# Kernel tuning notes

Hardware: AMD Instinct MI355X
Metric: run time of the kernel (lower is better)

Reference implementation:

```python
import jax, jax.numpy as jnp
import numpy as np

B, C, H, W = 4, 256, 64, 64
RED = 8
DQK = C // RED  # 32


def setup_inputs() -> dict:
    key = jax.random.key(0)
    ks = jax.random.split(key, 8)
    x = jax.random.normal(ks[0], (B, C, H, W), dtype=jnp.float32)
    # 1x1 conv weights == per-pixel linear maps: [out_ch, in_ch] + bias [out_ch]
    q_w = jax.random.normal(ks[1], (DQK, C), dtype=jnp.float32) * (1.0 / np.sqrt(C))
    q_b = jax.random.normal(ks[2], (DQK,), dtype=jnp.float32) * 0.01
    k_w = jax.random.normal(ks[3], (DQK, C), dtype=jnp.float32) * (1.0 / np.sqrt(C))
    k_b = jax.random.normal(ks[4], (DQK,), dtype=jnp.float32) * 0.01
    v_w = jax.random.normal(ks[5], (C, C), dtype=jnp.float32) * (1.0 / np.sqrt(C))
    v_b = jax.random.normal(ks[6], (C,), dtype=jnp.float32) * 0.01
    # gamma is init'd to 0 in torch; use a nonzero value so the attention path matters
    gamma = jax.random.normal(ks[7], (1,), dtype=jnp.float32) * 0.1
    return {"x": x, "q_w": q_w, "q_b": q_b, "k_w": k_w, "k_b": k_b,
            "v_w": v_w, "v_b": v_b, "gamma": gamma}


def reference(x, q_w, q_b, k_w, k_b, v_w, v_b, gamma):
    b, c, h, w = x.shape
    xf = x.reshape(b, c, h * w)  # [B, C, N]
    # 1x1 convs as channel matmuls
    q = jnp.einsum('dc,bcn->bdn', q_w, xf) + q_b[None, :, None]  # [B, DQK, N]
    k = jnp.einsum('dc,bcn->bdn', k_w, xf) + k_b[None, :, None]  # [B, DQK, N]
    v = jnp.einsum('oc,bcn->bon', v_w, xf) + v_b[None, :, None]  # [B, C, N]
    # attn[b, n, m] = softmax_m( q[:,n] . k[:,m] )  -- NO 1/sqrt(d) scale (faithful)
    scores = jnp.einsum('bdn,bdm->bnm', q, k)  # [B, N, N]
    attn = jax.nn.softmax(scores, axis=-1)
    # out = v @ attn^T : out[b, c, n] = sum_m v[b, c, m] * attn[b, n, m]
    out = jnp.einsum('bcm,bnm->bcn', v, attn).reshape(b, c, h, w)
    return gamma[0] * out + x
```

## Files before the change

kernel.cpp:

```cpp
#include <hip/hip_runtime.h>

#define NN 4096
#define CC 256
#define DQ 32

typedef __attribute__((ext_vector_type(8))) short short8;
typedef __attribute__((ext_vector_type(4))) float f32x4;

__device__ __forceinline__ unsigned short f32_to_bf16(float f) {
  unsigned int u = __float_as_uint(f);
  u += 0x7fffu + ((u >> 16) & 1u);
  return (unsigned short)(u >> 16);
}

__device__ __forceinline__ float bf16_to_f32(unsigned short u) {
  return __uint_as_float(((unsigned int)u) << 16);
}

__device__ __forceinline__ float exp2_hw(float f) {
  return __builtin_amdgcn_exp2f(f);
}

__device__ __forceinline__ unsigned cvt_pk_bf16(float lo, float hi) {
  unsigned r;
  asm("v_cvt_pk_bf16_f32 %0, %1, %2" : "=v"(r) : "v"(lo), "v"(hi));
  return r;
}

__device__ __forceinline__ void gld16(const void* g, void* l) {
  __builtin_amdgcn_global_load_lds(
      (__attribute__((address_space(1))) void*)(g),
      (__attribute__((address_space(3))) void*)(l), 16, 0, 0);
}

__global__ __launch_bounds__(256) void wconv_kernel(
    const float* qw, const float* kw, const float* vw,
    const float* qb, const float* kb, const float* vb,
    unsigned short* Wcat, float* bcat) {
  int id = blockIdx.x * 256 + threadIdx.x;
  if (id < 320 * 256) {
    int row = id >> 8;
    float v;
    if (row < 32) v = qw[id];
    else if (row < 64) v = kw[id - 32 * 256];
    else v = vw[id - 64 * 256];
    Wcat[id] = f32_to_bf16(v);
  }
  if (id < 320) {
    float v;
    if (id < 32) v = qb[id];
    else if (id < 64) v = kb[id - 32];
    else v = vb[id - 64];
    bcat[id] = v;
  }
}

__global__ __launch_bounds__(256, 2) void proj_kernel(
    const float* x, const unsigned short* Wcat, const float* bcat,
    unsigned short* Qt, unsigned short* Kt, unsigned short* V) {
  int bid = blockIdx.x;
  int b = bid >> 7, nb = bid & 127;
  int tid = threadIdx.x, lane = tid & 63, w = tid >> 6;
  int l15 = lane & 15, h = lane >> 4;

  __shared__ unsigned short xT[32][272];
  __shared__ unsigned short vbuf[CC][32];
  {
    const float* xb = x + (size_t)b * CC * NN + nb * 32;
    int c0 = tid >> 3, n4 = (tid & 7) * 4;
#pragma unroll
    for (int i = 0; i < 8; i++) {
      int c = c0 + i * 32;
      f32x4 v = *(const f32x4*)(xb + (size_t)c * NN + n4);
#pragma unroll
      for (int j = 0; j < 4; j++) xT[n4 + j][c] = f32_to_bf16(v[j]);
    }
  }
  __syncthreads();

  short8 af0[8], af1[8];
#pragma unroll
  for (int ks = 0; ks < 8; ks++) {
    af0[ks] = *(const short8*)(&xT[l15][ks * 32 + h * 8]);
    af1[ks] = *(const short8*)(&xT[16 + l15][ks * 32 + h * 8]);
  }

  f32x4 acc0[5], acc1[5];
#pragma unroll
  for (int t = 0; t < 5; t++)
#pragma unroll
    for (int r = 0; r < 4; r++) { acc0[t][r] = 0.f; acc1[t][r] = 0.f; }

#pragma unroll
  for (int ks = 0; ks < 8; ks++) {
#pragma unroll
    for (int d = 0; d < 5; d++) {
      int dt = w * 5 + d;
      short8 bfr = *(const short8*)(Wcat + (size_t)(dt * 16 + l15) * CC + ks * 32 + h * 8);
      acc0[d] = __builtin_amdgcn_mfma_f32_16x16x32_bf16(af0[ks], bfr, acc0[d], 0, 0, 0);
      acc1[d] = __builtin_amdgcn_mfma_f32_16x16x32_bf16(af1[ks], bfr, acc1[d], 0, 0, 0);
    }
  }

  unsigned short* Qtb = Qt + (size_t)b * NN * DQ;
  unsigned short* Ktb = Kt + (size_t)b * NN * DQ;
#pragma unroll
  for (int d = 0; d < 5; d++) {
    int dt = w * 5 + d;
    float bias = bcat[dt * 16 + l15];
    if (dt < 4) {
      float scale = dt < 2 ? 1.44269504f : 1.0f;
      unsigned short* dst = dt < 2 ? Qtb : Ktb;
      int dd = (dt & 1) * 16 + l15;
#pragma unroll
      for (int r = 0; r < 4; r++) {
        int nA = nb * 32 + h * 4 + r;
        dst[(size_t)nA * DQ + dd] = f32_to_bf16((acc0[d][r] + bias) * scale);
        dst[(size_t)(nA + 16) * DQ + dd] = f32_to_bf16((acc1[d][r] + bias) * scale);
      }
    } else {
      int c = (dt - 4) * 16 + l15;
#pragma unroll
      for (int r = 0; r < 4; r++) {
        vbuf[c][h * 4 + r] = f32_to_bf16(acc0[d][r] + bias);
        vbuf[c][16 + h * 4 + r] = f32_to_bf16(acc1[d][r] + bias);
      }
    }
  }
  __syncthreads();
  unsigned short* Vb = V + (size_t)b * CC * NN + nb * 32;
  int c = tid;
#pragma unroll
  for (int k = 0; k < 4; k++)
    *(f32x4*)(Vb + (size_t)c * NN + k * 8) = *(const f32x4*)(&vbuf[c][k * 8]);
}

__global__ __launch_bounds__(1024, 4) void attn_kernel(
    const unsigned short* Qt, const unsigned short* Kt, const unsigned short* V,
    unsigned short* Apart, float* rspart) {
  int bid = blockIdx.x;
  int b  = (bid & 7) >> 1;
  int mh = bid & 1;
  int nb = bid >> 3;
  int tid = threadIdx.x, lane = tid & 63, w = tid >> 6;
  int grp = w >> 3, wq = w & 7, wc = w & 3, ntb = (w >> 2) & 1;
  int l15 = lane & 15, h = lane >> 4;
  int n0 = nb * 128 + wq * 16;
  int m0base = mh * 2048;

  const unsigned short* Qtb = Qt + (size_t)b * NN * DQ;
  const unsigned short* Ktb = Kt + (size_t)b * NN * DQ;
  const unsigned short* Vb  = V  + (size_t)b * CC * NN;

  __shared__ __align__(16) char ldsb[139264];

  short8 qf = *(const short8*)(Qtb + (size_t)(n0 + l15) * DQ + h * 8);

  f32x4 acc[16];
#pragma unroll
  for (int t = 0; t < 16; t++)
#pragma unroll
    for (int r = 0; r < 4; r++) acc[t][r] = 0.f;
  float rs = 0.f;

  f32x4 zero4;
#pragma unroll
  for (int r = 0; r < 4; r++) zero4[r] = 0.f;

  auto stage_to = [&](char* dst, int T) {
    int m0 = m0base + T * 64;
#pragma unroll
    for (int it = 0; it < 2; it++) {
      int idx = it * 1024 + tid;
      int c = idx >> 3, sub = idx & 7;
      int moff = (sub ^ (c & 7)) * 8;
      gld16(Vb + (size_t)c * NN + m0 + moff, dst + idx * 16);
    }
  };

  short8 kA[2];
  auto kload = [&](int T) {
    int m0 = m0base + T * 64 + grp * 32;
#pragma unroll
    for (int s = 0; s < 2; s++)
      kA[s] = *(const short8*)(Ktb + (size_t)(m0 + s * 16 + l15) * DQ + h * 8);
  };

  auto pvstep = [&](const char* vb2, const char* prd) {
    const char* pb = prd + (grp * 8 + ntb * 4) * 1280 + l15 * 80 + h * 16;
    short8 pf0 = *(const short8*)(pb + 0 * 1280);
    short8 pf1 = *(const short8*)(pb + 1 * 1280);
    short8 pf2 = *(const short8*)(pb + 2 * 1280);
    short8 pf3 = *(const short8*)(pb + 3 * 1280);
#pragma unroll
    for (int ct = 0; ct < 4; ct++) {
      int c = wc * 64 + ct * 16 + l15;
      int sub = (grp * 4 + h) ^ (c & 7);
      short8 vf = *(const short8*)(vb2 + c * 128 + sub * 16);
      acc[ct * 4 + 0] = __builtin_amdgcn_mfma_f32_16x16x32_bf16(vf, pf0, acc[ct * 4 + 0], 0, 0, 0);
      acc[ct * 4 + 1] = __builtin_amdgcn_mfma_f32_16x16x32_bf16(vf, pf1, acc[ct * 4 + 1], 0, 0, 0);
      acc[ct * 4 + 2] = __builtin_amdgcn_mfma_f32_16x16x32_bf16(vf, pf2, acc[ct * 4 + 2], 0, 0, 0);
      acc[ct * 4 + 3] = __builtin_amdgcn_mfma_f32_16x16x32_bf16(vf, pf3, acc[ct * 4 + 3], 0, 0, 0);
    }
  };

  char* vpv  = ldsb + 2 * 32768;
  char* vrdy = ldsb + 0 * 32768;
  char* vstg = ldsb + 1 * 32768;
  char* pbw  = ldsb + 98304;
  char* pbr  = ldsb + 98304 + 20480;

  stage_to(vrdy, 0);
  kload(0);

  for (int T = 0; T < 32; T++) {
    if (T + 1 < 32) stage_to(vstg, T + 1);
    f32x4 st0 = __builtin_amdgcn_mfma_f32_16x16x32_bf16(kA[0], qf, zero4, 0, 0, 0);
    f32x4 st1 = __builtin_amdgcn_mfma_f32_16x16x32_bf16(kA[1], qf, zero4, 0, 0, 0);
    if (T + 1 < 32) kload(T + 1);
    if (T > 0) pvstep(vpv, pbr);
    float e0 = exp2_hw(st0[0]), e1 = exp2_hw(st0[1]);
    float e2 = exp2_hw(st0[2]), e3 = exp2_hw(st0[3]);
    float f0 = exp2_hw(st1[0]), f1 = exp2_hw(st1[1]);
    float f2 = exp2_hw(st1[2]), f3 = exp2_hw(st1[3]);
    rs += ((e0 + e1) + (e2 + e3)) + ((f0 + f1) + (f2 + f3));
    int2 q0, q1;
    q0.x = (int)cvt_pk_bf16(e0, e1); q0.y = (int)cvt_pk_bf16(e2, e3);
    q1.x = (int)cvt_pk_bf16(f0, f1); q1.y = (int)cvt_pk_bf16(f2, f3);
    {
      char* pw = pbw + w * 1280 + l15 * 80 + h * 8;
      *(int2*)(pw + 0)  = q0;
      *(int2*)(pw + 32) = q1;
    }
    asm volatile("s_waitcnt lgkmcnt(0)" ::: "memory");
    __builtin_amdgcn_s_barrier();
    asm volatile("" ::: "memory");
    char* t0 = vpv; vpv = vrdy; vrdy = vstg; vstg = t0;
    char* t1 = pbw; pbw = pbr; pbr = t1;
  }
  pvstep(vpv, pbr);

  rs += __shfl_xor(rs, 16);
  rs += __shfl_xor(rs, 32);
  if (h == 0)
    rspart[(size_t)(b * 4 + mh * 2 + grp) * NN + nb * 128 + wq * 16 + l15] = rs;

  __syncthreads();
  char* pregion = ldsb + 98304;
#pragma unroll
  for (int r = 0; r < 4; r++) {
    if (grp == 1) {
#pragma unroll
      for (int i = 0; i < 4; i++)
        *(f32x4*)(pregion + (w - 8) * 4096 + i * 1024 + lane * 16) = acc[r * 4 + i];
    }
    __syncthreads();
    if (grp == 0) {
#pragma unroll
      for (int i = 0; i < 4; i++) {
        f32x4 p = *(const f32x4*)(pregion + w * 4096 + i * 1024 + lane * 16);
#pragma unroll
        for (int q = 0; q < 4; q++) acc[r * 4 + i][q] += p[q];
      }
    }
    __syncthreads();
  }

  unsigned short* ldsus = (unsigned short*)ldsb;
  if (grp == 0) {
#pragma unroll
    for (int ct = 0; ct < 4; ct++)
#pragma unroll
      for (int i = 0; i < 4; i++)
#pragma unroll
        for (int r = 0; r < 4; r++) {
          int c = wc * 64 + ct * 16 + h * 4 + r;
          int n = (ntb * 4 + i) * 16 + l15;
          ldsus[c * 128 + n] = f32_to_bf16(acc[ct * 4 + i][r]);
        }
  }
  __syncthreads();
  {
    unsigned short* Adst = Apart + (size_t)(b * 2 + mh) * CC * NN + nb * 128;
    int c = tid >> 2, seg = tid & 3;
    const f32x4* src = (const f32x4*)(ldsb + c * 256 + seg * 64);
#pragma unroll
    for (int k = 0; k < 4; k++)
      *(f32x4*)(Adst + (size_t)c * NN + seg * 32 + k * 8) = src[k];
  }
}

__global__ __launch_bounds__(256) void fuse_kernel(
    const unsigned short* Apart, const float* rspart, const float* x,
    const float* gamma, float* out) {
  int bid = blockIdx.x;
  int b = bid >> 9, c = (bid >> 1) & 255, half = bid & 1;
  int n0 = half * 2048 + threadIdx.x * 8;

  short8 a0 = *(const short8*)(Apart + ((size_t)(b * 2 + 0) * CC + c) * NN + n0);
  short8 a1 = *(const short8*)(Apart + ((size_t)(b * 2 + 1) * CC + c) * NN + n0);

  const float* rp = rspart + (size_t)b * 4 * NN + n0;
  f32x4 rlo, rhi;
#pragma unroll
  for (int q = 0; q < 4; q++) { rlo[q] = 0.f; rhi[q] = 0.f; }
#pragma unroll
  for (int p = 0; p < 4; p++) {
    f32x4 ra = *(const f32x4*)(rp + (size_t)p * NN);
    f32x4 rb = *(const f32x4*)(rp + (size_t)p * NN + 4);
#pragma unroll
    for (int q = 0; q < 4; q++) { rlo[q] += ra[q]; rhi[q] += rb[q]; }
  }

  const float* xp = x + ((size_t)b * CC + c) * NN + n0;
  f32x4 x0 = *(const f32x4*)(xp), x1 = *(const f32x4*)(xp + 4);
  float g = gamma[0];

  f32x4 o0, o1;
#pragma unroll
  for (int q = 0; q < 4; q++) {
    float a = bf16_to_f32((unsigned short)a0[q]) + bf16_to_f32((unsigned short)a1[q]);
    o0[q] = g * a / rlo[q] + x0[q];
    float a2 = bf16_to_f32((unsigned short)a0[q + 4]) + bf16_to_f32((unsigned short)a1[q + 4]);
    o1[q] = g * a2 / rhi[q] + x1[q];
  }
  float* op = out + ((size_t)b * CC + c) * NN + n0;
  *(f32x4*)op = o0;
  *(f32x4*)(op + 4) = o1;
}

extern "C" void kernel_launch(void* const* d_in, const int* in_sizes, int n_in,
                              void* d_out, int out_size, void* d_ws, size_t ws_size,
                              hipStream_t stream) {
  (void)in_sizes; (void)n_in; (void)out_size; (void)ws_size;
  const float* x  = (const float*)d_in[0];
  const float* qw = (const float*)d_in[1];
  const float* qb = (const float*)d_in[2];
  const float* kw = (const float*)d_in[3];
  const float* kb = (const float*)d_in[4];
  const float* vw = (const float*)d_in[5];
  const float* vb = (const float*)d_in[6];
  const float* gamma = (const float*)d_in[7];
  float* out = (float*)d_out;

  char* ws = (char*)d_ws;
  unsigned short* Wcat  = (unsigned short*)(ws);
  float*          bcat  = (float*)(ws + 163840);
  unsigned short* Qt    = (unsigned short*)(ws + 165120);
  unsigned short* Kt    = (unsigned short*)(ws + 1213696);
  unsigned short* V     = (unsigned short*)(ws + 2262272);
  unsigned short* Apart = (unsigned short*)(ws + 10650880);
  float*          rsprt = (float*)(ws + 27428096);

  hipLaunchKernelGGL(wconv_kernel, dim3(320), dim3(256), 0, stream,
                     qw, kw, vw, qb, kb, vb, Wcat, bcat);
  hipLaunchKernelGGL(proj_kernel, dim3(512), dim3(256), 0, stream,
                     x, Wcat, bcat, Qt, Kt, V);
  hipLaunchKernelGGL(attn_kernel, dim3(256), dim3(1024), 0, stream,
                     Qt, Kt, V, Apart, rsprt);
  hipLaunchKernelGGL(fuse_kernel, dim3(2048), dim3(256), 0, stream,
                     Apart, rsprt, x, gamma, out);
}
```

Baseline: 96.48 us.

## Stage K tiles through LDS with async triple-buffering and swizzle P buffer

K fragments, previously read from global memory straight into registers each iteration, are now loaded asynchronously into a triple-buffered LDS ring two tiles ahead and then read from LDS. The P buffer drops its 80-byte padded rows for 64-byte rows with an XOR swizzle, and the PV step moves after the P write, with explicit vmcnt waits. The intent is to hide global K latency and avoid LDS bank conflicts at a smaller footprint. In exchange it uses more LDS and adds LDS reads plus precise wait-count bookkeeping.

```diff
diff --git a/kernel.cpp b/kernel.cpp
--- a/kernel.cpp
+++ b/kernel.cpp
@@ -152,7 +152,7 @@
   const unsigned short* Ktb = Kt + (size_t)b * NN * DQ;
   const unsigned short* Vb  = V  + (size_t)b * CC * NN;
 
-  __shared__ __align__(16) char ldsb[139264];
+  __shared__ __align__(16) char ldsb[143360];
 
   short8 qf = *(const short8*)(Qtb + (size_t)(n0 + l15) * DQ + h * 8);
 
@@ -167,31 +167,39 @@
 #pragma unroll
   for (int r = 0; r < 4; r++) zero4[r] = 0.f;
 
-  auto stage_to = [&](char* dst, int T) {
+  auto stage_v = [&](char* vdst, int T) {
     int m0 = m0base + T * 64;
 #pragma unroll
     for (int it = 0; it < 2; it++) {
       int idx = it * 1024 + tid;
       int c = idx >> 3, sub = idx & 7;
       int moff = (sub ^ (c & 7)) * 8;
-      gld16(Vb + (size_t)c * NN + m0 + moff, dst + idx * 16);
+      gld16(Vb + (size_t)c * NN + m0 + moff, vdst + idx * 16);
     }
   };
+  auto stage_k = [&](char* kdst, int T) {
+    int m0 = m0base + T * 64;
+    int r = w * 4 + (lane >> 2);
+    int lsl = (lane & 3) ^ ((lane >> 2) & 3);
+    if (lane < 16)
+      gld16(Ktb + (size_t)(m0 + r) * DQ + lsl * 8, kdst + w * 256 + lane * 16);
+  };
 
   short8 kA[2];
-  auto kload = [&](int T) {
-    int m0 = m0base + T * 64 + grp * 32;
-#pragma unroll
-    for (int s = 0; s < 2; s++)
-      kA[s] = *(const short8*)(Ktb + (size_t)(m0 + s * 16 + l15) * DQ + h * 8);
+  auto kload_lds = [&](const char* kb) {
+#pragma unroll
+    for (int s = 0; s < 2; s++) {
+      int row = grp * 32 + s * 16 + l15;
+      kA[s] = *(const short8*)(kb + row * 64 + ((h ^ (l15 & 3)) * 16));
+    }
   };
 
   auto pvstep = [&](const char* vb2, const char* prd) {
-    const char* pb = prd + (grp * 8 + ntb * 4) * 1280 + l15 * 80 + h * 16;
-    short8 pf0 = *(const short8*)(pb + 0 * 1280);
-    short8 pf1 = *(const short8*)(pb + 1 * 1280);
-    short8 pf2 = *(const short8*)(pb + 2 * 1280);
-    short8 pf3 = *(const short8*)(pb + 3 * 1280);
+    const char* pb = prd + (grp * 8 + ntb * 4) * 1024 + l15 * 64 + ((h ^ (l15 & 3)) * 16);
+    short8 pf0 = *(const short8*)(pb + 0 * 1024);
+    short8 pf1 = *(const short8*)(pb + 1 * 1024);
+    short8 pf2 = *(const short8*)(pb + 2 * 1024);
+    short8 pf3 = *(const short8*)(pb + 3 * 1024);
 #pragma unroll
     for (int ct = 0; ct < 4; ct++) {
       int c = wc * 64 + ct * 16 + l15;
@@ -207,18 +215,24 @@
   char* vpv  = ldsb + 2 * 32768;
   char* vrdy = ldsb + 0 * 32768;
   char* vstg = ldsb + 1 * 32768;
-  char* pbw  = ldsb + 98304;
-  char* pbr  = ldsb + 98304 + 20480;
-
-  stage_to(vrdy, 0);
-  kload(0);
+  char* kcur  = ldsb + 98304 + 0 * 4096;
+  char* knext = ldsb + 98304 + 1 * 4096;
+  char* kstg2 = ldsb + 98304 + 2 * 4096;
+  char* pbw  = ldsb + 110592;
+  char* pbr  = ldsb + 110592 + 16384;
+
+  stage_v(vrdy, 0);
+  stage_k(kcur, 0);
+  stage_k(knext, 1);
+  asm volatile("s_waitcnt vmcnt(0)" ::: "memory");
+  __syncthreads();
 
   for (int T = 0; T < 32; T++) {
-    if (T + 1 < 32) stage_to(vstg, T + 1);
+    kload_lds(kcur);
+    if (T + 1 < 32) stage_v(vstg, T + 1);
+    if (T + 2 < 32) stage_k(kstg2, T + 2);
     f32x4 st0 = __builtin_amdgcn_mfma_f32_16x16x32_bf16(kA[0], qf, zero4, 0, 0, 0);
     f32x4 st1 = __builtin_amdgcn_mfma_f32_16x16x32_bf16(kA[1], qf, zero4, 0, 0, 0);
-    if (T + 1 < 32) kload(T + 1);
-    if (T > 0) pvstep(vpv, pbr);
     float e0 = exp2_hw(st0[0]), e1 = exp2_hw(st0[1]);
     float e2 = exp2_hw(st0[2]), e3 = exp2_hw(st0[3]);
     float f0 = exp2_hw(st1[0]), f1 = exp2_hw(st1[1]);
@@ -228,15 +242,22 @@
     q0.x = (int)cvt_pk_bf16(e0, e1); q0.y = (int)cvt_pk_bf16(e2, e3);
     q1.x = (int)cvt_pk_bf16(f0, f1); q1.y = (int)cvt_pk_bf16(f2, f3);
     {
-      char* pw = pbw + w * 1280 + l15 * 80 + h * 8;
-      *(int2*)(pw + 0)  = q0;
-      *(int2*)(pw + 32) = q1;
-    }
+      char* pw = pbw + w * 1024 + l15 * 64;
+      int s0 = ((h >> 1) ^ (l15 & 3));
+      int s1 = ((2 + (h >> 1)) ^ (l15 & 3));
+      *(int2*)(pw + s0 * 16 + (h & 1) * 8) = q0;
+      *(int2*)(pw + s1 * 16 + (h & 1) * 8) = q1;
+    }
+    if (T > 0) pvstep(vpv, pbr);
+    if (T < 30)      asm volatile("s_waitcnt vmcnt(3)" ::: "memory");
+    else if (T == 30) asm volatile("s_waitcnt vmcnt(2)" ::: "memory");
+    else              asm volatile("s_waitcnt vmcnt(0)" ::: "memory");
     asm volatile("s_waitcnt lgkmcnt(0)" ::: "memory");
     __builtin_amdgcn_s_barrier();
     asm volatile("" ::: "memory");
     char* t0 = vpv; vpv = vrdy; vrdy = vstg; vstg = t0;
-    char* t1 = pbw; pbw = pbr; pbr = t1;
+    char* t1 = kcur; kcur = knext; knext = kstg2; kstg2 = t1;
+    char* t2 = pbw; pbw = pbr; pbr = t2;
   }
   pvstep(vpv, pbr);
 
@@ -246,7 +267,7 @@
     rspart[(size_t)(b * 4 + mh * 2 + grp) * NN + nb * 128 + wq * 16 + l15] = rs;
 
   __syncthreads();
-  char* pregion = ldsb + 98304;
+  char* pregion = ldsb + 110592;
 #pragma unroll
   for (int r = 0; r < 4; r++) {
     if (grp == 1) {
```

New measurement: 98.63 us. 1.02x slower.
